# Kernel tuning notes

Measured on AMD Instinct MI355X. Metric: run time of the kernel, lower is better.

## Reference

```python
import jax, jax.numpy as jnp
import numpy as np

DIM = 1024
NUM_HEADS = 16
HEAD_DIM = DIM // NUM_HEADS
REL_RANGE = 32
STM_REL_RANGE = 16  # hard-coded in the torch module (stm_vocab_size = 16*2+1)
STOK_VOCAB = 2 * REL_RANGE + 1
STM_VOCAB = 2 * STM_REL_RANGE + 1
NEG_INF = -1e18


def gen_rel_dist_matrix(n, rel_range, use_negative=True):
    idx = jnp.arange(n)
    d = idx[None, :] - idx[:, None]
    if use_negative:
        return jnp.clip(d, -rel_range, rel_range) + rel_range
    return jnp.clip(jnp.abs(d), 0, rel_range)


def setup_inputs() -> dict:
    key = jax.random.key(0)
    ks = jax.random.split(key, 10)
    B, STOK, STM = 8, 512, 128
    s = 0.02
    return {
        "stok_seq": jax.random.normal(ks[0], (B, STOK, DIM), jnp.float32),
        "stm_seq": jax.random.normal(ks[1], (B, STM, DIM), jnp.float32),
        "stok_pad_mask": jnp.zeros((B, 1, STOK), jnp.bool_),
        "stm_pad_mask": jnp.zeros((B, 1, STM), jnp.bool_),
        "qkv_w": jax.random.normal(ks[2], (3 * DIM, DIM), jnp.float32) * s,
        "qkv_b": jnp.zeros((3 * DIM,), jnp.float32),
        "out_w": jax.random.normal(ks[3], (DIM, DIM), jnp.float32) * s,
        "out_b": jnp.zeros((DIM,), jnp.float32),
        "rel_emb_k": jax.random.normal(ks[4], (STOK_VOCAB, HEAD_DIM), jnp.float32) * s,
        "rel_emb_v": jax.random.normal(ks[5], (STOK_VOCAB, HEAD_DIM), jnp.float32) * s,
        "stm_emb_k": jax.random.normal(ks[6], (STM_VOCAB, HEAD_DIM), jnp.float32) * s,
        "stm_emb_v": jax.random.normal(ks[7], (STM_VOCAB, HEAD_DIM), jnp.float32) * s,
    }


def reference(stok_seq, stm_seq, stok_pad_mask, stm_pad_mask,
              qkv_w, qkv_b, out_w, out_b,
              rel_emb_k, rel_emb_v, stm_emb_k, stm_emb_v):
    B, stok_len, _ = stok_seq.shape
    stm_len = stm_seq.shape[1]
    x = jnp.concatenate([stok_seq, stm_seq], axis=1)          # [B,S,D]
    mask = jnp.concatenate([stok_pad_mask, stm_pad_mask], axis=-1)  # [B,1,S]
    S = x.shape[1]

    qkv = (x @ qkv_w.T + qkv_b).reshape(B, S, 3, NUM_HEADS, HEAD_DIM)
    qkv = jnp.transpose(qkv, (2, 0, 3, 1, 4))                 # [3,B,H,S,hd]
    q, k, v = qkv[0], qkv[1], qkv[2]
    q = q / jnp.sqrt(jnp.float32(HEAD_DIM))

    # relative PE blocks (block-diagonal; cross blocks stay zero)
    stok_idx = gen_rel_dist_matrix(stok_len, REL_RANGE, True)
    stm_idx = gen_rel_dist_matrix(stm_len, STM_REL_RANGE, True)
    rel_pe_k = jnp.zeros((S, S, HEAD_DIM), jnp.float32)
    rel_pe_v = jnp.zeros((S, S, HEAD_DIM), jnp.float32)
    rel_pe_k = rel_pe_k.at[:stok_len, :stok_len].set(rel_emb_k[stok_idx])
    rel_pe_k = rel_pe_k.at[stok_len:, stok_len:].set(stm_emb_k[stm_idx])
    rel_pe_v = rel_pe_v.at[:stok_len, :stok_len].set(rel_emb_v[stok_idx])
    rel_pe_v = rel_pe_v.at[stok_len:, stok_len:].set(stm_emb_v[stm_idx])

    attn_score = jnp.einsum('bhqd,bhkd->bhqk', q, k)
    attn_score = attn_score + jnp.einsum('bhqd,qkd->bhqk', q, rel_pe_k)

    attn_score = jnp.where(mask[:, None, :, :], NEG_INF, attn_score)
    # block mask: statement queries cannot attend to sub-token keys
    attn_score = attn_score.at[:, :, stok_len:, :stok_len].set(NEG_INF)

    attn = jax.nn.softmax(attn_score, axis=-1)                # [B,H,S,S]
    context = jnp.einsum('bhqk,bhkd->bhqd', attn, v)
    context = context + jnp.einsum('bhqk,qkd->bhqd', attn, rel_pe_v)

    context = jnp.transpose(context, (0, 2, 1, 3)).reshape(B, S, DIM)
    final_output = context @ out_w.T + out_b
    return final_output, attn
```

## Files before the change

kernel.cpp:

```cpp
#include <hip/hip_runtime.h>
#include <stdint.h>

#define BB    8
#define HH    16
#define SS    640
#define STOK  512
#define STMN  128
#define HD    64
#define DIM   1024
#define NEGINF (-1e18f)

typedef short v8s __attribute__((ext_vector_type(8)));
typedef float v4f __attribute__((ext_vector_type(4)));

static __device__ __forceinline__ ushort f2b(float f) {
    union { float f; uint32_t u; } x; x.f = f;
    uint32_t u = (x.u + 0x7FFFu + ((x.u >> 16) & 1u)) >> 16;
    return (ushort)u;
}
static __device__ __forceinline__ float b2f(ushort h) {
    union { uint32_t u; float f; } x; x.u = ((uint32_t)h) << 16;
    return x.f;
}

static __device__ __forceinline__ void gld16(const ushort* g, ushort* l) {
    __builtin_amdgcn_global_load_lds(
        (const __attribute__((address_space(1))) unsigned int*)g,
        (__attribute__((address_space(3))) unsigned int*)l, 16, 0, 0);
}

__global__ __launch_bounds__(256) void cvt_bf16(
    const float* __restrict__ stok, const float* __restrict__ stm,
    const float* __restrict__ W, const float* __restrict__ Wo,
    ushort* __restrict__ xb, ushort* __restrict__ Wb,
    ushort* __restrict__ Woh, ushort* __restrict__ Wol)
{
    const int i = blockIdx.x * 256 + threadIdx.x;
    const int XG = 5120 * 256;
    const int WG = 3072 * 256;
    if (i < XG + WG) {
        float4 v; ushort* dst;
        if (i < XG) {
            int row = i >> 8, g = i & 255;
            int b = row / SS, s = row % SS;
            const float* src = (s < STOK)
                ? stok + ((size_t)b * STOK + s) * DIM
                : stm  + ((size_t)b * STMN + (s - STOK)) * DIM;
            v = *reinterpret_cast<const float4*>(src + g * 4);
            dst = xb + (size_t)row * DIM + g * 4;
        } else {
            int j = i - XG;
            int row = j >> 8, g = j & 255;
            v = *reinterpret_cast<const float4*>(W + (size_t)row * DIM + g * 4);
            dst = Wb + (size_t)row * DIM + g * 4;
        }
        ushort4 o;
        o.x = f2b(v.x); o.y = f2b(v.y); o.z = f2b(v.z); o.w = f2b(v.w);
        *reinterpret_cast<ushort4*>(dst) = o;
    } else {
        int j = i - XG - WG;
        int row = j >> 8, g = j & 255;
        float4 v = *reinterpret_cast<const float4*>(Wo + (size_t)row * DIM + g * 4);
        ushort4 hi, lo;
        hi.x = f2b(v.x); lo.x = f2b(v.x - b2f(hi.x));
        hi.y = f2b(v.y); lo.y = f2b(v.y - b2f(hi.y));
        hi.z = f2b(v.z); lo.z = f2b(v.z - b2f(hi.z));
        hi.w = f2b(v.w); lo.w = f2b(v.w - b2f(hi.w));
        *reinterpret_cast<ushort4*>(&Woh[(size_t)row * DIM + g * 4]) = hi;
        *reinterpret_cast<ushort4*>(&Wol[(size_t)row * DIM + g * 4]) = lo;
    }
}

__global__ __launch_bounds__(256) void gemm_qkv_mfma(
    const ushort* __restrict__ xb, const ushort* __restrict__ Wb,
    const float* __restrict__ bias,
    ushort* __restrict__ qb, ushort* __restrict__ kb, ushort* __restrict__ vtb)
{
    __shared__ __align__(16) ushort As[64 * 32];
    __shared__ __align__(16) ushort Bs[128 * 32];
    const int t = threadIdx.x, lane = t & 63, w = t >> 6;
    const int swz = ((blockIdx.x & 7) * 240) + (blockIdx.x >> 3);
    const int nt = swz / 80, mt = swz % 80;
    const int mb = mt * 64, nb = nt * 128;
    const int wm = (w >> 1) * 32, wn = (w & 1) * 64;
    const int lg = lane >> 4, lc = lane & 15;

    const int ra = t >> 2, pa = t & 3;
    const ushort* gA = xb + (size_t)(mb + ra) * DIM + (pa ^ ((ra >> 1) & 3)) * 8;
    ushort* lA = As + (w * 64) * 8;
    const ushort* gB[2]; ushort* lB[2];
#pragma unroll
    for (int i = 0; i < 2; ++i) {
        int c = t + i * 256, rb = c >> 2, pb = c & 3;
        gB[i] = Wb + (size_t)(nb + rb) * DIM + (pb ^ ((rb >> 1) & 3)) * 8;
        lB[i] = Bs + (i * 256 + w * 64) * 8;
    }

    v4f acc[2][4];
#pragma unroll
    for (int i = 0; i < 2; ++i)
#pragma unroll
        for (int j = 0; j < 4; ++j) acc[i][j] = (v4f){0.f, 0.f, 0.f, 0.f};

    for (int kt = 0; kt < 32; ++kt) {
        const int ko = kt * 32;
        __syncthreads();
        gld16(gA + ko, lA);
        gld16(gB[0] + ko, lB[0]);
        gld16(gB[1] + ko, lB[1]);
        __syncthreads();
        v8s af[2], bf[4];
#pragma unroll
        for (int i = 0; i < 2; ++i) {
            int ar = wm + i * 16 + lc;
            af[i] = *reinterpret_cast<const v8s*>(&As[ar * 32 + (lg ^ ((ar >> 1) & 3)) * 8]);
        }
#pragma unroll
        for (int j = 0; j < 4; ++j) {
            int br = wn + j * 16 + lc;
            bf[j] = *reinterpret_cast<const v8s*>(&Bs[br * 32 + (lg ^ ((br >> 1) & 3)) * 8]);
        }
#pragma unroll
        for (int i = 0; i < 2; ++i)
#pragma unroll
            for (int j = 0; j < 4; ++j)
                acc[i][j] = __builtin_amdgcn_mfma_f32_16x16x32_bf16(af[i], bf[j], acc[i][j], 0, 0, 0);
    }

    const int nregion = nb >> 10;
    if (nregion < 2) {
        ushort* dst = nregion ? kb : qb;
        const float scale = nregion ? 1.0f : 0.125f;
#pragma unroll
        for (int j = 0; j < 4; ++j) {
            int n = nb + wn + j * 16 + lc;
            int nn = n & 1023, h = nn >> 6, d = nn & 63;
            float bi = bias[n];
#pragma unroll
            for (int i = 0; i < 2; ++i) {
                int m0 = mb + wm + i * 16 + lg * 4;
                int b = m0 / SS, s0 = m0 % SS;
                size_t base = (((size_t)b * HH + h) * SS + s0) * HD + d;
#pragma unroll
                for (int r = 0; r < 4; ++r)
                    dst[base + (size_t)r * HD] = f2b((acc[i][j][r] + bi) * scale);
            }
        }
    } else {
#pragma unroll
        for (int j = 0; j < 4; ++j) {
            int n = nb + wn + j * 16 + lc;
            int nn = n & 1023, h = nn >> 6, d = nn & 63;
            float bi = bias[n];
#pragma unroll
            for (int i = 0; i < 2; ++i) {
                int m0 = mb + wm + i * 16 + lg * 4;
                int b = m0 / SS, s0 = m0 % SS;
                ushort4 pk;
                pk.x = f2b(acc[i][j][0] + bi);
                pk.y = f2b(acc[i][j][1] + bi);
                pk.z = f2b(acc[i][j][2] + bi);
                pk.w = f2b(acc[i][j][3] + bi);
                *reinterpret_cast<ushort4*>(
                    &vtb[(((size_t)b * HH + h) * HD + d) * SS + s0]) = pk;
            }
        }
    }
}

__global__ __launch_bounds__(256) void gemm_out_mfma(
    const ushort* __restrict__ Xh, const ushort* __restrict__ Xl,
    const ushort* __restrict__ Wh, const ushort* __restrict__ Wl,
    const float* __restrict__ bias, float* __restrict__ out)
{
    __shared__ __align__(16) ushort Ah[64 * 32];
    __shared__ __align__(16) ushort Al[64 * 32];
    __shared__ __align__(16) ushort Bh[64 * 32];
    __shared__ __align__(16) ushort Bl[64 * 32];
    const int t = threadIdx.x, lane = t & 63, w = t >> 6;
    const int swz = ((blockIdx.x & 7) * 160) + (blockIdx.x >> 3);
    const int nt = swz / 80, mt = swz % 80;
    const int mb = mt * 64, nb = nt * 64;
    const int wm = (w >> 1) * 32, wn = (w & 1) * 32;
    const int lg = lane >> 4, lc = lane & 15;

    const int rr = t >> 2, pp = t & 3;
    const size_t goff = (size_t)rr * DIM + (pp ^ ((rr >> 1) & 3)) * 8;
    const ushort* gAh = Xh + (size_t)mb * DIM + goff;
    const ushort* gAl = Xl + (size_t)mb * DIM + goff;
    const ushort* gBh = Wh + (size_t)nb * DIM + goff;
    const ushort* gBl = Wl + (size_t)nb * DIM + goff;
    const int wchunk = (w * 64) * 8;

    v4f acc[2][2];
#pragma unroll
    for (int i = 0; i < 2; ++i)
#pragma unroll
        for (int j = 0; j < 2; ++j) acc[i][j] = (v4f){0.f, 0.f, 0.f, 0.f};

    for (int kt = 0; kt < 32; ++kt) {
        const int ko = kt * 32;
        __syncthreads();
        gld16(gAh + ko, Ah + wchunk);
        gld16(gAl + ko, Al + wchunk);
        gld16(gBh + ko, Bh + wchunk);
        gld16(gBl + ko, Bl + wchunk);
        __syncthreads();
        v8s ahf[2], alf[2], bhf[2], blf[2];
#pragma unroll
        for (int i = 0; i < 2; ++i) {
            int ar = wm + i * 16 + lc;
            int ao = ar * 32 + (lg ^ ((ar >> 1) & 3)) * 8;
            ahf[i] = *reinterpret_cast<const v8s*>(&Ah[ao]);
            alf[i] = *reinterpret_cast<const v8s*>(&Al[ao]);
            int br = wn + i * 16 + lc;
            int bo = br * 32 + (lg ^ ((br >> 1) & 3)) * 8;
            bhf[i] = *reinterpret_cast<const v8s*>(&Bh[bo]);
            blf[i] = *reinterpret_cast<const v8s*>(&Bl[bo]);
        }
#pragma unroll
        for (int i = 0; i < 2; ++i)
#pragma unroll
            for (int j = 0; j < 2; ++j)
                acc[i][j] = __builtin_amdgcn_mfma_f32_16x16x32_bf16(ahf[i], bhf[j], acc[i][j], 0, 0, 0);
#pragma unroll
        for (int i = 0; i < 2; ++i)
#pragma unroll
            for (int j = 0; j < 2; ++j)
                acc[i][j] = __builtin_amdgcn_mfma_f32_16x16x32_bf16(alf[i], bhf[j], acc[i][j], 0, 0, 0);
#pragma unroll
        for (int i = 0; i < 2; ++i)
#pragma unroll
            for (int j = 0; j < 2; ++j)
                acc[i][j] = __builtin_amdgcn_mfma_f32_16x16x32_bf16(ahf[i], blf[j], acc[i][j], 0, 0, 0);
    }

#pragma unroll
    for (int j = 0; j < 2; ++j) {
        int n = nb + wn + j * 16 + lc;
        float bi = bias[n];
#pragma unroll
        for (int i = 0; i < 2; ++i) {
            int m0 = mb + wm + i * 16 + lg * 4;
#pragma unroll
            for (int r = 0; r < 4; ++r)
                out[(size_t)(m0 + r) * DIM + n] = acc[i][j][r] + bi;
        }
    }
}

__global__ __launch_bounds__(128) void attn_mfma(
    const ushort* __restrict__ qb, const ushort* __restrict__ kb,
    const ushort* __restrict__ vtb,
    const uint8_t* __restrict__ mtok, const uint8_t* __restrict__ mstm,
    const float* __restrict__ relk, const float* __restrict__ relv,
    const float* __restrict__ smk,  const float* __restrict__ smv,
    float* __restrict__ attn_out,
    ushort* __restrict__ ctxh, ushort* __restrict__ ctxl)
{
    __shared__ ushort qrel[32][72];
    __shared__ ushort Pfull[32][648];
    __shared__ ushort wbin[32][72];
    __shared__ float  linv[32];
    __shared__ float  ebuf[32];
    __shared__ uint64_t mlds[2][10];

    const int t    = threadIdx.x;
    const int lane = t & 63, w = t >> 6;
    const int swz  = ((blockIdx.x & 7) * 320) + (blockIdx.x >> 3);
    const int qt = swz % 20, bh = swz / 20;
    const int b = bh >> 4, h = bh & 15;
    const int qbase = qt * 32;
    const bool qstm = (qt >= 16);
    const size_t bhoff = (size_t)bh * (SS * HD);
    const int wq = w * 16, lg = lane >> 4, lc = lane & 15;
    const int RR = qstm ? 16 : 32;
    const int NV = qstm ? 33 : 65;
    const float* tabk = qstm ? smk : relk;

    for (int i = lane; i < 16 * 36; i += 64) {
        int r = i / 36, c = i - r * 36;
        *reinterpret_cast<uint32_t*>(&wbin[wq + r][c * 2]) = 0u;
    }

    if (lane < 10) {
        uint64_t m = 0;
        const int kb0 = lane * 64;
#pragma unroll
        for (int j = 0; j < 64; ++j) {
            int kg = kb0 + j;
            uint8_t mb = (kg < STOK) ? mtok[b * STOK + kg] : mstm[b * STMN + kg - STOK];
            m |= ((uint64_t)(mb ? 1u : 0u)) << j;
        }
        mlds[w][lane] = m;
    }

    const int qrow = qbase + wq + lc;
    v8s aq0 = *reinterpret_cast<const v8s*>(&qb[bhoff + (size_t)qrow * HD + lg * 8]);
    v8s aq1 = *reinterpret_cast<const v8s*>(&qb[bhoff + (size_t)qrow * HD + 32 + lg * 8]);

    {
        const int ndt = qstm ? 2 : 4;
        for (int dt = 0; dt < ndt; ++dt) {
            const float* rp = tabk + (size_t)(dt * 16 + lc) * HD;
            v8s bk0, bk1;
#pragma unroll
            for (int j = 0; j < 8; ++j) {
                bk0[j] = (short)f2b(rp[lg * 8 + j]);
                bk1[j] = (short)f2b(rp[32 + lg * 8 + j]);
            }
            v4f c4 = {0.f, 0.f, 0.f, 0.f};
            c4 = __builtin_amdgcn_mfma_f32_16x16x32_bf16(aq0, bk0, c4, 0, 0, 0);
            c4 = __builtin_amdgcn_mfma_f32_16x16x32_bf16(aq1, bk1, c4, 0, 0, 0);
#pragma unroll
            for (int r = 0; r < 4; ++r)
                qrel[wq + lg * 4 + r][dt * 16 + lc] = f2b(c4[r]);
        }
        const float* rp = tabk + (size_t)(NV - 1) * HD;
        float part = 0.f;
#pragma unroll
        for (int j = 0; j < 8; ++j) {
            part += b2f((ushort)aq0[j]) * rp[lg * 8 + j];
            part += b2f((ushort)aq1[j]) * rp[32 + lg * 8 + j];
        }
        part += __shfl_xor(part, 16);
        part += __shfl_xor(part, 32);
        if (lg == 0) qrel[wq + lc][NV - 1] = f2b(part);
    }

    const int gq = qbase + wq + lc;
    const float relLs = b2f(qrel[wq + lc][0]);
    const float relRs = b2f(qrel[wq + lc][2 * RR]);

    const int tile0 = qstm ? 8 : 0;
    float lsum1 = 0.f, e0 = 0.f, e1 = 0.f;
    v4f o[4];
#pragma unroll
    for (int dt = 0; dt < 4; ++dt) o[dt] = (v4f){0.f, 0.f, 0.f, 0.f};
    float* arow = attn_out + ((size_t)bh * SS + qbase) * SS;

    for (int kt = tile0; kt < 10; ++kt) {
        const ushort* kbase = kb + bhoff + (size_t)(kt * 64) * HD;
        const bool dorel = qstm || (kt < 8);
        const uint64_t mw = mlds[w][kt];
#pragma unroll
        for (int sub = 0; sub < 4; ++sub) {
            v8s bk0 = *reinterpret_cast<const v8s*>(&kbase[(sub * 16 + lc) * HD + lg * 8]);
            v8s bk1 = *reinterpret_cast<const v8s*>(&kbase[(sub * 16 + lc) * HD + 32 + lg * 8]);
            v4f c4 = {0.f, 0.f, 0.f, 0.f};
            c4 = __builtin_amdgcn_mfma_f32_16x16x32_bf16(bk0, aq0, c4, 0, 0, 0);
            c4 = __builtin_amdgcn_mfma_f32_16x16x32_bf16(bk1, aq1, c4, 0, 0, 0);
            const int kgb = kt * 64 + sub * 16 + lg * 4;
            float p4[4];
#pragma unroll
            for (int r = 0; r < 4; ++r) {
                int kg = kgb + r;
                int dlt = kg - gq;
                bool inband = dorel && (dlt > -RR) && (dlt < RR);
                float val = c4[r];
                if (dorel) {
                    float rv;
                    if (inband) rv = b2f(qrel[wq + lc][dlt + RR]);
                    else        rv = (dlt <= -RR) ? relLs : relRs;
                    val += rv;
                }
                if ((mw >> (sub * 16 + lg * 4 + r)) & 1) val = NEGINF;
                float p = __expf(val);
                lsum1 += p;
                p4[r] = p;
                if (inband) wbin[wq + lc][dlt + RR] = f2b(p);
                else if (dorel) {
                    if (dlt <= -RR) e0 += p;
                    else            e1 += p;
                }
            }
            uint32_t lo = (uint32_t)f2b(p4[0]) | ((uint32_t)f2b(p4[1]) << 16);
            uint32_t hi = (uint32_t)f2b(p4[2]) | ((uint32_t)f2b(p4[3]) << 16);
            uint64_t pk64 = (uint64_t)lo | ((uint64_t)hi << 32);
            *reinterpret_cast<uint64_t*>(&Pfull[wq + lc][kgb]) = pk64;
        }
        v8s ap0 = *reinterpret_cast<const v8s*>(&Pfull[wq + lc][kt * 64 + lg * 8]);
        v8s ap1 = *reinterpret_cast<const v8s*>(&Pfull[wq + lc][kt * 64 + 32 + lg * 8]);
        const ushort* vbase = vtb + bhoff + kt * 64;
#pragma unroll
        for (int dt = 0; dt < 4; ++dt) {
            v8s bv0 = *reinterpret_cast<const v8s*>(&vbase[(size_t)(dt * 16 + lc) * SS + lg * 8]);
            v8s bv1 = *reinterpret_cast<const v8s*>(&vbase[(size_t)(dt * 16 + lc) * SS + 32 + lg * 8]);
            o[dt] = __builtin_amdgcn_mfma_f32_16x16x32_bf16(ap0, bv0, o[dt], 0, 0, 0);
            o[dt] = __builtin_amdgcn_mfma_f32_16x16x32_bf16(ap1, bv1, o[dt], 0, 0, 0);
        }
    }

    {
        float s = lsum1;
        s += __shfl_xor(s, 16); s += __shfl_xor(s, 32);
        float e0s = e0;
        e0s += __shfl_xor(e0s, 16); e0s += __shfl_xor(e0s, 32);
        float e1s = e1;
        e1s += __shfl_xor(e1s, 16); e1s += __shfl_xor(e1s, 32);
        if (lg == 0) {
            linv[wq + lc] = 1.f / s;
            ebuf[wq + lc] = e1s;
            wbin[wq + lc][0] = f2b(e0s);
            if (qstm) wbin[wq + lc][32] = f2b(e1s);
        }
    }

#pragma unroll
    for (int rr = 0; rr < 4; ++rr) {
        int row = wq + rr * 4 + lg;
        float iv = linv[row];
        float* rowp = arow + (size_t)row * SS;
        if (qstm) {
            v4f z = (v4f){0.f, 0.f, 0.f, 0.f};
#pragma unroll
            for (int kt = 0; kt < 8; ++kt)
                __builtin_nontemporal_store(z,
                    reinterpret_cast<v4f*>(&rowp[kt * 64 + lc * 4]));
#pragma unroll
            for (int kt = 8; kt < 10; ++kt) {
                ushort4 pk = *reinterpret_cast<ushort4*>(&Pfull[row][kt * 64 + lc * 4]);
                v4f pv4;
                pv4[0] = b2f(pk.x) * iv;
                pv4[1] = b2f(pk.y) * iv;
                pv4[2] = b2f(pk.z) * iv;
                pv4[3] = b2f(pk.w) * iv;
                __builtin_nontemporal_store(pv4,
                    reinterpret_cast<v4f*>(&rowp[kt * 64 + lc * 4]));
            }
        } else {
#pragma unroll
            for (int kt = 0; kt < 10; ++kt) {
                ushort4 pk = *reinterpret_cast<ushort4*>(&Pfull[row][kt * 64 + lc * 4]);
                v4f pv4;
                pv4[0] = b2f(pk.x) * iv;
                pv4[1] = b2f(pk.y) * iv;
                pv4[2] = b2f(pk.z) * iv;
                pv4[3] = b2f(pk.w) * iv;
                __builtin_nontemporal_store(pv4,
                    reinterpret_cast<v4f*>(&rowp[kt * 64 + lc * 4]));
            }
        }
    }

    __syncthreads();
    {
        ushort* Rv = &Pfull[0][0];
        const float* tabv = qstm ? smv : relv;
        for (int idx = t; idx < 64 * 64; idx += 128) {
            int d = idx >> 6, v = idx & 63;
            float f = (v < NV) ? tabv[(size_t)v * HD + d] : 0.f;
            Rv[d * 72 + v] = f2b(f);
        }
    }
    __syncthreads();
    {
        const ushort* Rv = &Pfull[0][0];
        v8s aw0 = *reinterpret_cast<const v8s*>(&wbin[wq + lc][lg * 8]);
        v8s aw1 = *reinterpret_cast<const v8s*>(&wbin[wq + lc][32 + lg * 8]);
#pragma unroll
        for (int dt = 0; dt < 4; ++dt) {
            v8s bv0 = *reinterpret_cast<const v8s*>(&Rv[(dt * 16 + lc) * 72 + lg * 8]);
            v8s bv1 = *reinterpret_cast<const v8s*>(&Rv[(dt * 16 + lc) * 72 + 32 + lg * 8]);
            o[dt] = __builtin_amdgcn_mfma_f32_16x16x32_bf16(aw0, bv0, o[dt], 0, 0, 0);
            o[dt] = __builtin_amdgcn_mfma_f32_16x16x32_bf16(aw1, bv1, o[dt], 0, 0, 0);
        }
        if (!qstm) {
#pragma unroll
            for (int r = 0; r < 4; ++r) {
                float e1r = ebuf[wq + lg * 4 + r];
#pragma unroll
                for (int dt = 0; dt < 4; ++dt)
                    o[dt][r] += e1r * relv[(size_t)64 * HD + dt * 16 + lc];
            }
        }
    }

    float invr[4];
#pragma unroll
    for (int r = 0; r < 4; ++r) invr[r] = linv[wq + lg * 4 + r];
#pragma unroll
    for (int dt = 0; dt < 4; ++dt)
#pragma unroll
        for (int r = 0; r < 4; ++r) {
            int gq2 = qbase + wq + lg * 4 + r;
            size_t idx = ((size_t)b * SS + gq2) * DIM + h * HD + dt * 16 + lc;
            float v = o[dt][r] * invr[r];
            ushort hi = f2b(v);
            ctxh[idx] = hi;
            ctxl[idx] = f2b(v - b2f(hi));
        }
}

extern "C" void kernel_launch(void* const* d_in, const int* in_sizes, int n_in,
                              void* d_out, int out_size, void* d_ws, size_t ws_size,
                              hipStream_t stream)
{
    const float*   stok  = (const float*)d_in[0];
    const float*   stm   = (const float*)d_in[1];
    const uint8_t* mtok  = (const uint8_t*)d_in[2];
    const uint8_t* mstm  = (const uint8_t*)d_in[3];
    const float*   qkv_w = (const float*)d_in[4];
    const float*   qkv_b = (const float*)d_in[5];
    const float*   out_w = (const float*)d_in[6];
    const float*   out_b = (const float*)d_in[7];
    const float*   relk  = (const float*)d_in[8];
    const float*   relv  = (const float*)d_in[9];
    const float*   smk   = (const float*)d_in[10];
    const float*   smv   = (const float*)d_in[11];

    float* out_final = (float*)d_out;
    float* out_attn  = out_final + (size_t)BB * SS * DIM;

    const size_t SZ = (size_t)BB * HH * SS * HD;
    ushort* qb16 = (ushort*)d_ws;
    ushort* kb16 = qb16 + SZ;
    ushort* vt16 = kb16 + SZ;
    ushort* xb16 = vt16 + SZ;
    ushort* wb16 = xb16 + SZ;
    ushort* ctxh = wb16 + (size_t)3 * DIM * DIM;
    ushort* ctxl = ctxh + SZ;
    ushort* woh  = ctxl + SZ;
    ushort* wol  = woh + (size_t)DIM * DIM;

    cvt_bf16<<<dim3(9216), dim3(256), 0, stream>>>(stok, stm, qkv_w, out_w,
                                                   xb16, wb16, woh, wol);
    gemm_qkv_mfma<<<dim3(1920), dim3(256), 0, stream>>>(xb16, wb16, qkv_b, qb16, kb16, vt16);
    attn_mfma<<<dim3(2560), dim3(128), 0, stream>>>(qb16, kb16, vt16, mtok, mstm,
                                                    relk, relv, smk, smv, out_attn, ctxh, ctxl);
    gemm_out_mfma<<<dim3(1280), dim3(256), 0, stream>>>(ctxh, ctxl, woh, wol, out_b, out_final);
}
```

Measured before the change: 297.6 us.

## Split attention key tiles across two wave pairs per block

```diff
diff --git a/kernel.cpp b/kernel.cpp
--- a/kernel.cpp
+++ b/kernel.cpp
@@ -249,7 +249,7 @@
     }
 }
 
-__global__ __launch_bounds__(128) void attn_mfma(
+__global__ __launch_bounds__(256) void attn_mfma(
     const ushort* __restrict__ qb, const ushort* __restrict__ kb,
     const ushort* __restrict__ vtb,
     const uint8_t* __restrict__ mtok, const uint8_t* __restrict__ mstm,
@@ -259,47 +259,50 @@
     ushort* __restrict__ ctxh, ushort* __restrict__ ctxl)
 {
     __shared__ ushort qrel[32][72];
-    __shared__ ushort Pfull[32][648];
+    __shared__ __align__(16) ushort Pfull[32][648];
     __shared__ ushort wbin[32][72];
     __shared__ float  linv[32];
     __shared__ float  ebuf[32];
-    __shared__ uint64_t mlds[2][10];
+    __shared__ float  pl[2][32], pe0[2][32], pe1[2][32];
+    __shared__ uint64_t mlds[10];
 
     const int t    = threadIdx.x;
     const int lane = t & 63, w = t >> 6;
+    const int rh = w & 1, th = w >> 1;
     const int swz  = ((blockIdx.x & 7) * 320) + (blockIdx.x >> 3);
     const int qt = swz % 20, bh = swz / 20;
     const int b = bh >> 4, h = bh & 15;
     const int qbase = qt * 32;
     const bool qstm = (qt >= 16);
     const size_t bhoff = (size_t)bh * (SS * HD);
-    const int wq = w * 16, lg = lane >> 4, lc = lane & 15;
+    const int wq = rh * 16, lg = lane >> 4, lc = lane & 15;
     const int RR = qstm ? 16 : 32;
     const int NV = qstm ? 33 : 65;
     const float* tabk = qstm ? smk : relk;
 
-    for (int i = lane; i < 16 * 36; i += 64) {
-        int r = i / 36, c = i - r * 36;
-        *reinterpret_cast<uint32_t*>(&wbin[wq + r][c * 2]) = 0u;
-    }
-
-    if (lane < 10) {
+    if (w < 2)
+        for (int i = lane; i < 16 * 36; i += 64) {
+            int r = i / 36, c = i - r * 36;
+            *reinterpret_cast<uint32_t*>(&wbin[wq + r][c * 2]) = 0u;
+        }
+
+    if (t < 10) {
         uint64_t m = 0;
-        const int kb0 = lane * 64;
+        const int kb0 = t * 64;
 #pragma unroll
         for (int j = 0; j < 64; ++j) {
             int kg = kb0 + j;
             uint8_t mb = (kg < STOK) ? mtok[b * STOK + kg] : mstm[b * STMN + kg - STOK];
             m |= ((uint64_t)(mb ? 1u : 0u)) << j;
         }
-        mlds[w][lane] = m;
+        mlds[t] = m;
     }
 
     const int qrow = qbase + wq + lc;
     v8s aq0 = *reinterpret_cast<const v8s*>(&qb[bhoff + (size_t)qrow * HD + lg * 8]);
     v8s aq1 = *reinterpret_cast<const v8s*>(&qb[bhoff + (size_t)qrow * HD + 32 + lg * 8]);
 
-    {
+    if (w < 2) {
         const int ndt = qstm ? 2 : 4;
         for (int dt = 0; dt < ndt; ++dt) {
             const float* rp = tabk + (size_t)(dt * 16 + lc) * HD;
@@ -327,22 +330,26 @@
         part += __shfl_xor(part, 32);
         if (lg == 0) qrel[wq + lc][NV - 1] = f2b(part);
     }
+    __syncthreads();
 
     const int gq = qbase + wq + lc;
     const float relLs = b2f(qrel[wq + lc][0]);
     const float relRs = b2f(qrel[wq + lc][2 * RR]);
 
     const int tile0 = qstm ? 8 : 0;
+    const int tcnt = (10 - tile0) >> 1;
+    const int tstart = tile0 + th * tcnt, tend = tstart + tcnt;
+
     float lsum1 = 0.f, e0 = 0.f, e1 = 0.f;
     v4f o[4];
 #pragma unroll
     for (int dt = 0; dt < 4; ++dt) o[dt] = (v4f){0.f, 0.f, 0.f, 0.f};
     float* arow = attn_out + ((size_t)bh * SS + qbase) * SS;
 
-    for (int kt = tile0; kt < 10; ++kt) {
+    for (int kt = tstart; kt < tend; ++kt) {
         const ushort* kbase = kb + bhoff + (size_t)(kt * 64) * HD;
         const bool dorel = qstm || (kt < 8);
-        const uint64_t mw = mlds[w][kt];
+        const uint64_t mw = mlds[kt];
 #pragma unroll
         for (int sub = 0; sub < 4; ++sub) {
             v8s bk0 = *reinterpret_cast<const v8s*>(&kbase[(sub * 16 + lc) * HD + lg * 8]);
@@ -399,16 +406,28 @@
         float e1s = e1;
         e1s += __shfl_xor(e1s, 16); e1s += __shfl_xor(e1s, 32);
         if (lg == 0) {
-            linv[wq + lc] = 1.f / s;
-            ebuf[wq + lc] = e1s;
-            wbin[wq + lc][0] = f2b(e0s);
-            if (qstm) wbin[wq + lc][32] = f2b(e1s);
-        }
-    }
-
-#pragma unroll
-    for (int rr = 0; rr < 4; ++rr) {
-        int row = wq + rr * 4 + lg;
+            pl[th][wq + lc]  = s;
+            pe0[th][wq + lc] = e0s;
+            pe1[th][wq + lc] = e1s;
+        }
+    }
+    __syncthreads();
+
+    if (t < 32) {
+        int row = t;
+        float ls = pl[0][row] + pl[1][row];
+        linv[row] = 1.f / ls;
+        float e0s = pe0[0][row] + pe0[1][row];
+        float e1s = pe1[0][row] + pe1[1][row];
+        ebuf[row] = e1s;
+        wbin[row][0] = f2b(e0s);
+        if (qstm) wbin[row][32] = f2b(e1s);
+    }
+    __syncthreads();
+
+#pragma unroll
+    for (int rr = 0; rr < 2; ++rr) {
+        int row = w * 8 + rr * 4 + lg;
         float iv = linv[row];
         float* rowp = arow + (size_t)row * SS;
         if (qstm) {
@@ -442,19 +461,34 @@
             }
         }
     }
-
     __syncthreads();
+
+    float* ob = reinterpret_cast<float*>(&Pfull[0][0] + 16384);
+    if (w >= 2) {
+#pragma unroll
+        for (int dt = 0; dt < 4; ++dt)
+#pragma unroll
+            for (int r = 0; r < 4; ++r)
+                ob[(wq + lg * 4 + r) * 64 + dt * 16 + lc] = o[dt][r];
+    }
     {
         ushort* Rv = &Pfull[0][0];
         const float* tabv = qstm ? smv : relv;
-        for (int idx = t; idx < 64 * 64; idx += 128) {
+        for (int idx = t; idx < 64 * 64; idx += 256) {
             int d = idx >> 6, v = idx & 63;
             float f = (v < NV) ? tabv[(size_t)v * HD + d] : 0.f;
             Rv[d * 72 + v] = f2b(f);
         }
     }
     __syncthreads();
-    {
+
+    if (w < 2) {
+#pragma unroll
+        for (int dt = 0; dt < 4; ++dt)
+#pragma unroll
+            for (int r = 0; r < 4; ++r)
+                o[dt][r] += ob[(wq + lg * 4 + r) * 64 + dt * 16 + lc];
+
         const ushort* Rv = &Pfull[0][0];
         v8s aw0 = *reinterpret_cast<const v8s*>(&wbin[wq + lc][lg * 8]);
         v8s aw1 = *reinterpret_cast<const v8s*>(&wbin[wq + lc][32 + lg * 8]);
@@ -474,22 +508,22 @@
                     o[dt][r] += e1r * relv[(size_t)64 * HD + dt * 16 + lc];
             }
         }
-    }
-
-    float invr[4];
-#pragma unroll
-    for (int r = 0; r < 4; ++r) invr[r] = linv[wq + lg * 4 + r];
-#pragma unroll
-    for (int dt = 0; dt < 4; ++dt)
-#pragma unroll
-        for (int r = 0; r < 4; ++r) {
-            int gq2 = qbase + wq + lg * 4 + r;
-            size_t idx = ((size_t)b * SS + gq2) * DIM + h * HD + dt * 16 + lc;
-            float v = o[dt][r] * invr[r];
-            ushort hi = f2b(v);
-            ctxh[idx] = hi;
-            ctxl[idx] = f2b(v - b2f(hi));
-        }
+
+        float invr[4];
+#pragma unroll
+        for (int r = 0; r < 4; ++r) invr[r] = linv[wq + lg * 4 + r];
+#pragma unroll
+        for (int dt = 0; dt < 4; ++dt)
+#pragma unroll
+            for (int r = 0; r < 4; ++r) {
+                int gq2 = qbase + wq + lg * 4 + r;
+                size_t idx = ((size_t)b * SS + gq2) * DIM + h * HD + dt * 16 + lc;
+                float v = o[dt][r] * invr[r];
+                ushort hi = f2b(v);
+                ctxh[idx] = hi;
+                ctxl[idx] = f2b(v - b2f(hi));
+            }
+    }
 }
 
 extern "C" void kernel_launch(void* const* d_in, const int* in_sizes, int n_in,
@@ -526,7 +560,7 @@
     cvt_bf16<<<dim3(9216), dim3(256), 0, stream>>>(stok, stm, qkv_w, out_w,
                                                    xb16, wb16, woh, wol);
     gemm_qkv_mfma<<<dim3(1920), dim3(256), 0, stream>>>(xb16, wb16, qkv_b, qb16, kb16, vt16);
-    attn_mfma<<<dim3(2560), dim3(128), 0, stream>>>(qb16, kb16, vt16, mtok, mstm,
+    attn_mfma<<<dim3(2560), dim3(256), 0, stream>>>(qb16, kb16, vt16, mtok, mstm,
                                                     relk, relv, smk, smv, out_attn, ctxh, ctxl);
     gemm_out_mfma<<<dim3(1280), dim3(256), 0, stream>>>(ctxh, ctxl, woh, wol, out_b, out_final);
 }
```

Result: faster. 263.7 us (-11.4%).
